# Kernel optimization log

Hardware: AMD Instinct MI355X
Metric: run time of the kernel (lower is better)

The kernel has to match this reference:

```python
import jax, jax.numpy as jnp
import numpy as np

N_ITER = 3  # GenSP(n_iter=3)


def _gen_sp(x, stoken):
    """Faithful JAX port of ssn_iter + visualize_spixels (GenSP.forward).

    Instead of materializing the dense (B,S,P) affinity via sparse_coo->to_dense,
    we keep the exact 9-candidate structure: each pixel has 9 candidate
    superpixels (its init superpixel and 8 grid neighbors). The bmm-based
    centroid update is mathematically identical to a masked segment-sum over
    those candidates, and the dense argmax over S equals the argmax over the 9
    candidates (all other columns are exactly 0).
    """
    B, C, H, W = x.shape
    sh = sw = stoken
    nsh, nsw = H // sh, W // sw
    S = nsh * nsw          # number of superpixels
    P = H * W              # number of pixels

    xs = jax.lax.stop_gradient(x)  # torch runs all SSN iterations under no_grad

    # adaptive_avg_pool2d with exact divisibility == block mean
    cent = xs.reshape(B, C, nsh, sh, nsw, sw).mean(axis=(3, 5)).reshape(B, C, S)  # (B,C,S)

    # nearest-neighbor upsampled init label map (B-independent)
    lab = jnp.arange(S, dtype=jnp.int32).reshape(nsh, nsw)
    lab = jnp.repeat(jnp.repeat(lab, sh, axis=0), sw, axis=1).reshape(P)  # (P,)
    lx, ly = lab % nsw, lab // nsw

    offs = [(dy, dx) for dy in (-1, 0, 1) for dx in (-1, 0, 1)]  # matches r-nsw, r, r+nsw ordering
    cand = jnp.stack([lab + dy * nsw + dx for dy, dx in offs])   # (9,P) candidate spixel ids
    valid = jnp.stack([(lx + dx >= 0) & (lx + dx < nsw) &
                       (ly + dy >= 0) & (ly + dy < nsh) for dy, dx in offs])  # (9,P)
    cand_safe = jnp.where(valid, cand, 0)

    px = xs.reshape(B, C, P).transpose(0, 2, 1)  # (B,P,C)

    def affinity(cent_b, px_b):
        # PairwiseDistFunction: squared L2 pixel->candidate centroid, inf if invalid
        ct = cent_b.T  # (S,C)
        d = jnp.stack([jnp.sum((px_b - ct[cand_safe[k]]) ** 2, axis=-1)
                       for k in range(9)])             # (9,P)
        logits = jnp.where(valid, -d, -jnp.inf)
        return jnp.where(valid, jax.nn.softmax(logits, axis=0), 0.0)  # (9,P)

    def centroid_update(aff, px_b):
        # == bmm(abs_affinity, px) / abs_affinity.sum(2), via segment sums
        num = jnp.zeros((S, C), px_b.dtype)
        den = jnp.zeros((S,), px_b.dtype)
        for k in range(9):
            num = num + jax.ops.segment_sum(aff[k][:, None] * px_b, cand_safe[k], num_segments=S)
            den = den + jax.ops.segment_sum(aff[k], cand_safe[k], num_segments=S)
        return (num / (den[:, None] + 1e-16)).T  # (C,S)

    def hard_labels(cent_b, px_b):
        c = cent_b
        for _ in range(N_ITER - 1):
            c = centroid_update(affinity(c, px_b), px_b)
        aff = affinity(c, px_b)                         # final abs_affinity (sparse form)
        best = jnp.argmax(aff, axis=0)                  # (P,)
        return jnp.take_along_axis(cand_safe, best[None], axis=0)[0]

    labels = jax.vmap(hard_labels)(cent, px)[0]         # torch paints only image[0]

    # visualize_spixels: per-superpixel per-channel mean, painted back
    px0 = x[0].reshape(C, P).T                          # (P,C), grads flow here
    sums = jax.ops.segment_sum(px0, labels, num_segments=S)
    cnt = jax.ops.segment_sum(jnp.ones((P,), px0.dtype), labels, num_segments=S)
    means = sums / jnp.maximum(cnt, 1.0)[:, None]       # (S,C)
    return means[labels].T.reshape(1, C, H, W)


def setup_inputs() -> dict:
    key = jax.random.key(0)
    x = jax.random.normal(key, (1, 64, 384, 384), dtype=jnp.float32)
    return {"x": x, "stoken": 16}


def reference(x, stoken):
    return _gen_sp(x, stoken)
```

## Files before the change

kernel.cpp:

```cpp
#include <hip/hip_runtime.h>
#include <math.h>


#define NC   64
#define IMW  384
#define HWP  (384*384)
#define NSH  24
#define NSW  24
#define NS   (NSH*NSW)
#define NBG  (NS*4)

__global__ __launch_bounds__(256) void k_cent_part(const float* __restrict__ x,
                                                   double* __restrict__ centp) {
    int bg = blockIdx.x, b = bg >> 2, g = bg & 3;
    int by = b / NSW, bx = b % NSW;
    int t = threadIdx.x, q = t >> 2, r = t & 3;
    const float* gp = x + (size_t)q * HWP + (size_t)(by * 16 + g * 4) * IMW + bx * 16 + r * 4;
    double s = 0.0;
    #pragma unroll
    for (int j = 0; j < 4; ++j) {
        float4 v = *(const float4*)(gp + (size_t)j * IMW);
        s += (double)v.x; s += (double)v.y; s += (double)v.z; s += (double)v.w;
    }
    s += __shfl_xor(s, 1, 64);
    s += __shfl_xor(s, 2, 64);
    if (r == 0) centp[(size_t)bg * NC + q] = s;
}

__global__ __launch_bounds__(64) void k_cent_red(const double* __restrict__ centp,
                                                 double* __restrict__ cent,
                                                 double* __restrict__ cnorm) {
    int s = blockIdx.x, c = threadIdx.x;
    double v = centp[(size_t)(s * 4 + 0) * NC + c] + centp[(size_t)(s * 4 + 1) * NC + c]
             + centp[(size_t)(s * 4 + 2) * NC + c] + centp[(size_t)(s * 4 + 3) * NC + c];
    v *= (1.0 / 256.0);
    cent[s * NC + c] = v;
    double n2 = v * v;
    #pragma unroll
    for (int off = 32; off >= 1; off >>= 1) n2 += __shfl_down(n2, off, 64);
    if (c == 0) cnorm[s] = n2;
}

__global__ __launch_bounds__(64) void k_iter(const float* __restrict__ x,
        const double* __restrict__ cent, const double* __restrict__ cnorm,
        double* __restrict__ bnum, double* __restrict__ bden) {
    int bg = blockIdx.x, b = bg >> 2, g = bg & 3;
    int by = b / NSW, bx = b % NSW;
    int t = threadIdx.x;
    __shared__ double aff[9][66];

    int cand[9]; bool vld[9];
    #pragma unroll
    for (int k = 0; k < 9; ++k) {
        int cy = by + k / 3 - 1, cx = bx + k % 3 - 1;
        vld[k] = (cy >= 0) && (cy < NSH) && (cx >= 0) && (cx < NSW);
        cand[k] = vld[k] ? (cy * NSW + cx) : 0;
    }

    const float* xp = x + (size_t)(by * 16 + g * 4 + (t >> 4)) * IMW + bx * 16 + (t & 15);
    double dot[9] = {0, 0, 0, 0, 0, 0, 0, 0, 0};
    #pragma unroll 4
    for (int c = 0; c < NC; ++c) {
        double xv = (double)xp[(size_t)c * HWP];
        #pragma unroll
        for (int k = 0; k < 9; ++k)
            dot[k] = fma(xv, cent[(size_t)cand[k] * NC + c], dot[k]);
    }
    double d[9], m = -1e300;
    #pragma unroll
    for (int k = 0; k < 9; ++k) {
        d[k] = fma(dot[k], -2.0, cnorm[cand[k]]);
        if (vld[k]) m = fmax(m, -d[k]);
    }
    double e[9], ss = 0.0;
    #pragma unroll
    for (int k = 0; k < 9; ++k) { e[k] = vld[k] ? exp(-d[k] - m) : 0.0; ss += e[k]; }
    double inv = 1.0 / ss;
    #pragma unroll
    for (int k = 0; k < 9; ++k) { e[k] *= inv; aff[k][t] = e[k]; }

    #pragma unroll
    for (int k = 0; k < 9; ++k) {
        double dn = e[k];
        #pragma unroll
        for (int off = 32; off >= 1; off >>= 1) dn += __shfl_down(dn, off, 64);
        if (t == 0) bden[(size_t)bg * 9 + k] = dn;
    }
    __syncthreads();

    int c = t;
    double acc[9] = {0, 0, 0, 0, 0, 0, 0, 0, 0};
    const float* xq = x + (size_t)c * HWP + (size_t)(by * 16 + g * 4) * IMW + bx * 16;
    for (int r = 0; r < 4; ++r) {
        #pragma unroll
        for (int q = 0; q < 4; ++q) {
            float4 xv = *(const float4*)(xq + (size_t)r * IMW + q * 4);
            int pp = r * 16 + q * 4;
            #pragma unroll
            for (int k = 0; k < 9; ++k) {
                acc[k] = fma(aff[k][pp + 0], (double)xv.x, acc[k]);
                acc[k] = fma(aff[k][pp + 1], (double)xv.y, acc[k]);
                acc[k] = fma(aff[k][pp + 2], (double)xv.z, acc[k]);
                acc[k] = fma(aff[k][pp + 3], (double)xv.w, acc[k]);
            }
        }
    }
    #pragma unroll
    for (int k = 0; k < 9; ++k) bnum[((size_t)bg * 9 + k) * NC + c] = acc[k];
}

__global__ __launch_bounds__(64) void k_gather_cent(const double* __restrict__ bnum,
                                                    const double* __restrict__ bden,
                                                    double* __restrict__ cent,
                                                    double* __restrict__ cnorm) {
    int s = blockIdx.x, c = threadIdx.x;
    int sy = s / NSW, sx = s % NSW;
    double num = 0.0, den = 0.0;
    #pragma unroll
    for (int k = 0; k < 9; ++k) {
        int by2 = sy - (k / 3 - 1), bx2 = sx - (k % 3 - 1);
        if (by2 >= 0 && by2 < NSH && bx2 >= 0 && bx2 < NSW) {
            int b2 = by2 * NSW + bx2;
            #pragma unroll
            for (int g = 0; g < 4; ++g) {
                int bg = b2 * 4 + g;
                num += bnum[((size_t)bg * 9 + k) * NC + c];
                den += bden[(size_t)bg * 9 + k];
            }
        }
    }
    double v = num / (den + 1e-16);
    cent[s * NC + c] = v;
    double n2 = v * v;
    #pragma unroll
    for (int off = 32; off >= 1; off >>= 1) n2 += __shfl_down(n2, off, 64);
    if (c == 0) cnorm[s] = n2;
}

__global__ __launch_bounds__(64) void k_final(const float* __restrict__ x,
        const double* __restrict__ cent, const double* __restrict__ cnorm,
        int* __restrict__ labels,
        double* __restrict__ bnum, double* __restrict__ bden) {
    int bg = blockIdx.x, b = bg >> 2, g = bg & 3;
    int by = b / NSW, bx = b % NSW;
    int t = threadIdx.x;
    __shared__ double aff[9][66];

    int cand[9]; bool vld[9];
    #pragma unroll
    for (int k = 0; k < 9; ++k) {
        int cy = by + k / 3 - 1, cx = bx + k % 3 - 1;
        vld[k] = (cy >= 0) && (cy < NSH) && (cx >= 0) && (cx < NSW);
        cand[k] = vld[k] ? (cy * NSW + cx) : 0;
    }

    const float* xp = x + (size_t)(by * 16 + g * 4 + (t >> 4)) * IMW + bx * 16 + (t & 15);
    double dot[9] = {0, 0, 0, 0, 0, 0, 0, 0, 0};
    #pragma unroll 4
    for (int c = 0; c < NC; ++c) {
        double xv = (double)xp[(size_t)c * HWP];
        #pragma unroll
        for (int k = 0; k < 9; ++k)
            dot[k] = fma(xv, cent[(size_t)cand[k] * NC + c], dot[k]);
    }
    double bestd = 1e300; int bk = 0;
    #pragma unroll
    for (int k = 0; k < 9; ++k) {
        double dv = fma(dot[k], -2.0, cnorm[cand[k]]);
        if (vld[k] && dv < bestd) { bestd = dv; bk = k; }
    }
    labels[(size_t)(by * 16 + g * 4 + (t >> 4)) * IMW + bx * 16 + (t & 15)] =
        (by + bk / 3 - 1) * NSW + (bx + bk % 3 - 1);
    #pragma unroll
    for (int k = 0; k < 9; ++k) aff[k][t] = (bk == k) ? 1.0 : 0.0;

    #pragma unroll
    for (int k = 0; k < 9; ++k) {
        int cnt = (bk == k);
        #pragma unroll
        for (int off = 32; off >= 1; off >>= 1) cnt += __shfl_down(cnt, off, 64);
        if (t == 0) bden[(size_t)bg * 9 + k] = (double)cnt;
    }
    __syncthreads();

    int c = t;
    double acc[9] = {0, 0, 0, 0, 0, 0, 0, 0, 0};
    const float* xq = x + (size_t)c * HWP + (size_t)(by * 16 + g * 4) * IMW + bx * 16;
    for (int r = 0; r < 4; ++r) {
        #pragma unroll
        for (int q = 0; q < 4; ++q) {
            float4 xv = *(const float4*)(xq + (size_t)r * IMW + q * 4);
            int pp = r * 16 + q * 4;
            #pragma unroll
            for (int k = 0; k < 9; ++k) {
                acc[k] = fma(aff[k][pp + 0], (double)xv.x, acc[k]);
                acc[k] = fma(aff[k][pp + 1], (double)xv.y, acc[k]);
                acc[k] = fma(aff[k][pp + 2], (double)xv.z, acc[k]);
                acc[k] = fma(aff[k][pp + 3], (double)xv.w, acc[k]);
            }
        }
    }
    #pragma unroll
    for (int k = 0; k < 9; ++k) bnum[((size_t)bg * 9 + k) * NC + c] = acc[k];
}

__global__ __launch_bounds__(64) void k_means_(const double* __restrict__ bnum,
                                               const double* __restrict__ bden,
                                               float* __restrict__ means) {
    int s = blockIdx.x, c = threadIdx.x;
    int sy = s / NSW, sx = s % NSW;
    double num = 0.0, den = 0.0;
    #pragma unroll
    for (int k = 0; k < 9; ++k) {
        int by2 = sy - (k / 3 - 1), bx2 = sx - (k % 3 - 1);
        if (by2 >= 0 && by2 < NSH && bx2 >= 0 && bx2 < NSW) {
            int b2 = by2 * NSW + bx2;
            #pragma unroll
            for (int g = 0; g < 4; ++g) {
                int bg = b2 * 4 + g;
                num += bnum[((size_t)bg * 9 + k) * NC + c];
                den += bden[(size_t)bg * 9 + k];
            }
        }
    }
    means[s * NC + c] = (float)(num / fmax(den, 1.0));
}

__global__ __launch_bounds__(256) void k_paint(const int* __restrict__ labels,
                                               const float* __restrict__ means,
                                               float* __restrict__ out) {
    int p0 = (blockIdx.x * 256 + threadIdx.x) * 4;
    int4 lb = *(const int4*)&labels[p0];
    int c0 = blockIdx.y * 4;
    #pragma unroll
    for (int j = 0; j < 4; ++j) {
        int c = c0 + j;
        float4 o;
        o.x = means[lb.x * NC + c];
        o.y = means[lb.y * NC + c];
        o.z = means[lb.z * NC + c];
        o.w = means[lb.w * NC + c];
        *(float4*)&out[(size_t)c * HWP + p0] = o;
    }
}

extern "C" void kernel_launch(void* const* d_in, const int* in_sizes, int n_in,
                              void* d_out, int out_size, void* d_ws, size_t ws_size,
                              hipStream_t stream) {
    const float* x = (const float*)d_in[0];
    float* out = (float*)d_out;
    char* ws = (char*)d_ws;
    char* od = (char*)d_out;

    constexpr size_t CENTP_B = (size_t)NBG * NC * 8;
    constexpr size_t CENT_B  = (size_t)NS * NC * 8;
    constexpr size_t CNRM_B  = (size_t)NS * 8;
    constexpr size_t BNUM_B  = (size_t)NBG * 9 * NC * 8;
    constexpr size_t BDEN_B  = (size_t)NBG * 9 * 8;
    constexpr size_t LAB_B   = (size_t)HWP * 4;
    constexpr size_t MEANS_B = (size_t)NS * NC * 4;
    constexpr size_t T_PAINT = LAB_B + MEANS_B;
    constexpr size_t T_CENT  = T_PAINT + 2 * (CENT_B + CNRM_B);
    constexpr size_t T_ALL   = T_CENT + CENTP_B + BNUM_B + BDEN_B;

    int* labels = (int*)ws;
    float* means = (float*)(ws + LAB_B);
    double *centA, *centB, *cnormA, *cnormB, *centp, *bnum, *bden;
    if (ws_size >= T_ALL) {
        centA  = (double*)(ws + T_PAINT);
        centB  = (double*)(ws + T_PAINT + CENT_B);
        cnormA = (double*)(ws + T_PAINT + 2 * CENT_B);
        cnormB = (double*)(ws + T_PAINT + 2 * CENT_B + CNRM_B);
        centp  = (double*)(ws + T_CENT);
        bnum   = (double*)(ws + T_CENT + CENTP_B);
        bden   = (double*)(ws + T_CENT + CENTP_B + BNUM_B);
    } else if (ws_size >= T_CENT) {
        centA  = (double*)(ws + T_PAINT);
        centB  = (double*)(ws + T_PAINT + CENT_B);
        cnormA = (double*)(ws + T_PAINT + 2 * CENT_B);
        cnormB = (double*)(ws + T_PAINT + 2 * CENT_B + CNRM_B);
        centp  = (double*)od;
        bnum   = (double*)(od + CENTP_B);
        bden   = (double*)(od + CENTP_B + BNUM_B);
    } else {
        centp  = (double*)od;
        bnum   = (double*)(od + CENTP_B);
        bden   = (double*)(od + CENTP_B + BNUM_B);
        centA  = (double*)(od + CENTP_B + BNUM_B + BDEN_B);
        centB  = (double*)(od + CENTP_B + BNUM_B + BDEN_B + CENT_B);
        cnormA = (double*)(od + CENTP_B + BNUM_B + BDEN_B + 2 * CENT_B);
        cnormB = (double*)(od + CENTP_B + BNUM_B + BDEN_B + 2 * CENT_B + CNRM_B);
    }

    k_cent_part<<<NBG, 256, 0, stream>>>(x, centp);
    k_cent_red<<<NS, 64, 0, stream>>>(centp, centA, cnormA);
    k_iter<<<NBG, 64, 0, stream>>>(x, centA, cnormA, bnum, bden);
    k_gather_cent<<<NS, 64, 0, stream>>>(bnum, bden, centB, cnormB);
    k_iter<<<NBG, 64, 0, stream>>>(x, centB, cnormB, bnum, bden);
    k_gather_cent<<<NS, 64, 0, stream>>>(bnum, bden, centA, cnormA);
    k_final<<<NBG, 64, 0, stream>>>(x, centA, cnormA, labels, bnum, bden);
    k_means_<<<NS, 64, 0, stream>>>(bnum, bden, means);
    k_paint<<<dim3(HWP / 1024, NC / 4), 256, 0, stream>>>(labels, means, out);
}
```

Measured before the change: 136.0 us.

## Split iter/final kernels across four waves with shared-memory x tile reuse

Both the iteration kernel and the final-assignment kernel now run four wavefronts per block instead of one. The channel dot-product loop is split across the waves, and the partial dots are combined through shared memory. Each wave caches its x values in a padded LDS tile, so the centroid-numerator pass reads x from shared memory instead of reloading it from global memory, and that pass is split across waves by candidate pairs. This aims to raise parallelism and cut redundant global traffic, at the cost of extra LDS use, two barriers, and softmax work that runs on a single wave.

Result: slower. 148.8 us (+9.5%).

```diff
diff --git a/kernel.cpp b/kernel.cpp
--- a/kernel.cpp
+++ b/kernel.cpp
@@ -41,13 +41,19 @@
     if (c == 0) cnorm[s] = n2;
 }
 
-__global__ __launch_bounds__(64) void k_iter(const float* __restrict__ x,
+__global__ __launch_bounds__(256, 5) void k_iter(const float* __restrict__ x,
         const double* __restrict__ cent, const double* __restrict__ cnorm,
         double* __restrict__ bnum, double* __restrict__ bden) {
     int bg = blockIdx.x, b = bg >> 2, g = bg & 3;
     int by = b / NSW, bx = b % NSW;
     int t = threadIdx.x;
-    __shared__ double aff[9][66];
+    int p = t & 63;
+    int q = __builtin_amdgcn_readfirstlane(t >> 6);
+
+    __shared__ float  xb[64 * 65];
+    __shared__ double pdot_aff[3 * 9 * 64];
+    double* pdot = pdot_aff;
+    double* aff  = pdot_aff;
 
     int cand[9]; bool vld[9];
     #pragma unroll
@@ -57,56 +63,63 @@
         cand[k] = vld[k] ? (cy * NSW + cx) : 0;
     }
 
-    const float* xp = x + (size_t)(by * 16 + g * 4 + (t >> 4)) * IMW + bx * 16 + (t & 15);
+    const float* xp = x + (size_t)(by * 16 + g * 4 + (p >> 4)) * IMW + bx * 16 + (p & 15);
     double dot[9] = {0, 0, 0, 0, 0, 0, 0, 0, 0};
-    #pragma unroll 4
-    for (int c = 0; c < NC; ++c) {
-        double xv = (double)xp[(size_t)c * HWP];
+    #pragma unroll
+    for (int i = 0; i < 16; ++i) {
+        int c = q * 16 + i;
+        float xf = xp[(size_t)c * HWP];
+        xb[p * 65 + c] = xf;
+        double xv = (double)xf;
         #pragma unroll
         for (int k = 0; k < 9; ++k)
             dot[k] = fma(xv, cent[(size_t)cand[k] * NC + c], dot[k]);
     }
-    double d[9], m = -1e300;
-    #pragma unroll
-    for (int k = 0; k < 9; ++k) {
-        d[k] = fma(dot[k], -2.0, cnorm[cand[k]]);
-        if (vld[k]) m = fmax(m, -d[k]);
-    }
-    double e[9], ss = 0.0;
-    #pragma unroll
-    for (int k = 0; k < 9; ++k) { e[k] = vld[k] ? exp(-d[k] - m) : 0.0; ss += e[k]; }
-    double inv = 1.0 / ss;
-    #pragma unroll
-    for (int k = 0; k < 9; ++k) { e[k] *= inv; aff[k][t] = e[k]; }
-
-    #pragma unroll
-    for (int k = 0; k < 9; ++k) {
-        double dn = e[k];
-        #pragma unroll
-        for (int off = 32; off >= 1; off >>= 1) dn += __shfl_down(dn, off, 64);
-        if (t == 0) bden[(size_t)bg * 9 + k] = dn;
+    if (q) {
+        #pragma unroll
+        for (int k = 0; k < 9; ++k) pdot[((q - 1) * 9 + k) * 64 + p] = dot[k];
     }
     __syncthreads();
 
-    int c = t;
-    double acc[9] = {0, 0, 0, 0, 0, 0, 0, 0, 0};
-    const float* xq = x + (size_t)c * HWP + (size_t)(by * 16 + g * 4) * IMW + bx * 16;
-    for (int r = 0; r < 4; ++r) {
-        #pragma unroll
-        for (int q = 0; q < 4; ++q) {
-            float4 xv = *(const float4*)(xq + (size_t)r * IMW + q * 4);
-            int pp = r * 16 + q * 4;
+    if (q == 0) {
+        double d[9], m = -1e300;
+        #pragma unroll
+        for (int k = 0; k < 9; ++k) {
+            double dt = dot[k] + pdot[(0 * 9 + k) * 64 + p]
+                               + pdot[(1 * 9 + k) * 64 + p]
+                               + pdot[(2 * 9 + k) * 64 + p];
+            d[k] = fma(dt, -2.0, cnorm[cand[k]]);
+            if (vld[k]) m = fmax(m, -d[k]);
+        }
+        double e[9], ss = 0.0;
+        #pragma unroll
+        for (int k = 0; k < 9; ++k) { e[k] = vld[k] ? exp(-d[k] - m) : 0.0; ss += e[k]; }
+        double inv = 1.0 / ss;
+        #pragma unroll
+        for (int k = 0; k < 9; ++k) { e[k] *= inv; aff[p * 10 + k] = e[k]; }
+        #pragma unroll
+        for (int k = 0; k < 9; ++k) {
+            double dn = e[k];
             #pragma unroll
-            for (int k = 0; k < 9; ++k) {
-                acc[k] = fma(aff[k][pp + 0], (double)xv.x, acc[k]);
-                acc[k] = fma(aff[k][pp + 1], (double)xv.y, acc[k]);
-                acc[k] = fma(aff[k][pp + 2], (double)xv.z, acc[k]);
-                acc[k] = fma(aff[k][pp + 3], (double)xv.w, acc[k]);
-            }
-        }
-    }
-    #pragma unroll
-    for (int k = 0; k < 9; ++k) bnum[((size_t)bg * 9 + k) * NC + c] = acc[k];
+            for (int off = 32; off >= 1; off >>= 1) dn += __shfl_down(dn, off, 64);
+            if (p == 0) bden[(size_t)bg * 9 + k] = dn;
+        }
+    }
+    __syncthreads();
+
+    int c = t & 63, kq = t >> 6;
+    int k0 = 2 * kq;
+    double a0 = 0, a1 = 0, a2 = 0;
+    for (int pp = 0; pp < 64; ++pp) {
+        double xd = (double)xb[pp * 65 + c];
+        double2 av = *(const double2*)&aff[pp * 10 + k0];
+        a0 = fma(av.x, xd, a0);
+        a1 = fma(av.y, xd, a1);
+        if (kq == 0) a2 = fma(aff[pp * 10 + 8], xd, a2);
+    }
+    bnum[((size_t)bg * 9 + k0) * NC + c] = a0;
+    bnum[((size_t)bg * 9 + k0 + 1) * NC + c] = a1;
+    if (kq == 0) bnum[((size_t)bg * 9 + 8) * NC + c] = a2;
 }
 
 __global__ __launch_bounds__(64) void k_gather_cent(const double* __restrict__ bnum,
@@ -137,14 +150,20 @@
     if (c == 0) cnorm[s] = n2;
 }
 
-__global__ __launch_bounds__(64) void k_final(const float* __restrict__ x,
+__global__ __launch_bounds__(256, 5) void k_final(const float* __restrict__ x,
         const double* __restrict__ cent, const double* __restrict__ cnorm,
         int* __restrict__ labels,
         double* __restrict__ bnum, double* __restrict__ bden) {
     int bg = blockIdx.x, b = bg >> 2, g = bg & 3;
     int by = b / NSW, bx = b % NSW;
     int t = threadIdx.x;
-    __shared__ double aff[9][66];
+    int p = t & 63;
+    int q = __builtin_amdgcn_readfirstlane(t >> 6);
+
+    __shared__ float  xb[64 * 65];
+    __shared__ double pdot_aff[3 * 9 * 64];
+    double* pdot = pdot_aff;
+    int* ibk = (int*)pdot_aff;
 
     int cand[9]; bool vld[9];
     #pragma unroll
@@ -154,54 +173,60 @@
         cand[k] = vld[k] ? (cy * NSW + cx) : 0;
     }
 
-    const float* xp = x + (size_t)(by * 16 + g * 4 + (t >> 4)) * IMW + bx * 16 + (t & 15);
+    const float* xp = x + (size_t)(by * 16 + g * 4 + (p >> 4)) * IMW + bx * 16 + (p & 15);
     double dot[9] = {0, 0, 0, 0, 0, 0, 0, 0, 0};
-    #pragma unroll 4
-    for (int c = 0; c < NC; ++c) {
-        double xv = (double)xp[(size_t)c * HWP];
+    #pragma unroll
+    for (int i = 0; i < 16; ++i) {
+        int c = q * 16 + i;
+        float xf = xp[(size_t)c * HWP];
+        xb[p * 65 + c] = xf;
+        double xv = (double)xf;
         #pragma unroll
         for (int k = 0; k < 9; ++k)
             dot[k] = fma(xv, cent[(size_t)cand[k] * NC + c], dot[k]);
     }
-    double bestd = 1e300; int bk = 0;
-    #pragma unroll
-    for (int k = 0; k < 9; ++k) {
-        double dv = fma(dot[k], -2.0, cnorm[cand[k]]);
-        if (vld[k] && dv < bestd) { bestd = dv; bk = k; }
-    }
-    labels[(size_t)(by * 16 + g * 4 + (t >> 4)) * IMW + bx * 16 + (t & 15)] =
-        (by + bk / 3 - 1) * NSW + (bx + bk % 3 - 1);
-    #pragma unroll
-    for (int k = 0; k < 9; ++k) aff[k][t] = (bk == k) ? 1.0 : 0.0;
-
-    #pragma unroll
-    for (int k = 0; k < 9; ++k) {
-        int cnt = (bk == k);
-        #pragma unroll
-        for (int off = 32; off >= 1; off >>= 1) cnt += __shfl_down(cnt, off, 64);
-        if (t == 0) bden[(size_t)bg * 9 + k] = (double)cnt;
+    if (q) {
+        #pragma unroll
+        for (int k = 0; k < 9; ++k) pdot[((q - 1) * 9 + k) * 64 + p] = dot[k];
     }
     __syncthreads();
 
-    int c = t;
-    double acc[9] = {0, 0, 0, 0, 0, 0, 0, 0, 0};
-    const float* xq = x + (size_t)c * HWP + (size_t)(by * 16 + g * 4) * IMW + bx * 16;
-    for (int r = 0; r < 4; ++r) {
-        #pragma unroll
-        for (int q = 0; q < 4; ++q) {
-            float4 xv = *(const float4*)(xq + (size_t)r * IMW + q * 4);
-            int pp = r * 16 + q * 4;
+    if (q == 0) {
+        double bestd = 1e300; int bk = 0;
+        #pragma unroll
+        for (int k = 0; k < 9; ++k) {
+            double dt = dot[k] + pdot[(0 * 9 + k) * 64 + p]
+                               + pdot[(1 * 9 + k) * 64 + p]
+                               + pdot[(2 * 9 + k) * 64 + p];
+            double dv = fma(dt, -2.0, cnorm[cand[k]]);
+            if (vld[k] && dv < bestd) { bestd = dv; bk = k; }
+        }
+        ibk[p] = bk;
+        labels[(size_t)(by * 16 + g * 4 + (p >> 4)) * IMW + bx * 16 + (p & 15)] =
+            (by + bk / 3 - 1) * NSW + (bx + bk % 3 - 1);
+        #pragma unroll
+        for (int k = 0; k < 9; ++k) {
+            int cnt = (bk == k);
             #pragma unroll
-            for (int k = 0; k < 9; ++k) {
-                acc[k] = fma(aff[k][pp + 0], (double)xv.x, acc[k]);
-                acc[k] = fma(aff[k][pp + 1], (double)xv.y, acc[k]);
-                acc[k] = fma(aff[k][pp + 2], (double)xv.z, acc[k]);
-                acc[k] = fma(aff[k][pp + 3], (double)xv.w, acc[k]);
-            }
-        }
-    }
-    #pragma unroll
-    for (int k = 0; k < 9; ++k) bnum[((size_t)bg * 9 + k) * NC + c] = acc[k];
+            for (int off = 32; off >= 1; off >>= 1) cnt += __shfl_down(cnt, off, 64);
+            if (p == 0) bden[(size_t)bg * 9 + k] = (double)cnt;
+        }
+    }
+    __syncthreads();
+
+    int c = t & 63, kq = t >> 6;
+    int k0 = 2 * kq;
+    double a0 = 0, a1 = 0, a2 = 0;
+    for (int pp = 0; pp < 64; ++pp) {
+        int bkp = ibk[pp];
+        double xd = (double)xb[pp * 65 + c];
+        a0 += (bkp == k0) ? xd : 0.0;
+        a1 += (bkp == k0 + 1) ? xd : 0.0;
+        if (kq == 0) a2 += (bkp == 8) ? xd : 0.0;
+    }
+    bnum[((size_t)bg * 9 + k0) * NC + c] = a0;
+    bnum[((size_t)bg * 9 + k0 + 1) * NC + c] = a1;
+    if (kq == 0) bnum[((size_t)bg * 9 + 8) * NC + c] = a2;
 }
 
 __global__ __launch_bounds__(64) void k_means_(const double* __restrict__ bnum,
@@ -294,11 +319,11 @@
 
     k_cent_part<<<NBG, 256, 0, stream>>>(x, centp);
     k_cent_red<<<NS, 64, 0, stream>>>(centp, centA, cnormA);
-    k_iter<<<NBG, 64, 0, stream>>>(x, centA, cnormA, bnum, bden);
+    k_iter<<<NBG, 256, 0, stream>>>(x, centA, cnormA, bnum, bden);
     k_gather_cent<<<NS, 64, 0, stream>>>(bnum, bden, centB, cnormB);
-    k_iter<<<NBG, 64, 0, stream>>>(x, centB, cnormB, bnum, bden);
+    k_iter<<<NBG, 256, 0, stream>>>(x, centB, cnormB, bnum, bden);
     k_gather_cent<<<NS, 64, 0, stream>>>(bnum, bden, centA, cnormA);
-    k_final<<<NBG, 64, 0, stream>>>(x, centA, cnormA, labels, bnum, bden);
+    k_final<<<NBG, 256, 0, stream>>>(x, centA, cnormA, labels, bnum, bden);
     k_means_<<<NS, 64, 0, stream>>>(bnum, bden, means);
     k_paint<<<dim3(HWP / 1024, NC / 4), 256, 0, stream>>>(labels, means, out);
 }
```
